# Kernel optimization log

Hardware: AMD Instinct MI355X
Metric: run time of the kernel (lower is better)

The kernel has to match this reference:

```python
import jax, jax.numpy as jnp
import numpy as np

NODES_PER_GRAPH = 116
HEADS = 2
D_HEAD = 116  # out_channels per head
HID = 256
B = 512
N = B * NODES_PER_GRAPH
DEG = 8
E = N * DEG
D_OUT = HEADS * D_HEAD  # 232


def setup_inputs() -> dict:
    key = jax.random.key(0)
    ks = jax.random.split(key, 6)
    h_flat = jax.random.normal(ks[0], (N, HID), dtype=jnp.float32)
    # every node receives DEG edges from random nodes within its own 116-node graph
    dst = jnp.repeat(jnp.arange(N, dtype=jnp.int64), DEG)
    offs = jax.random.randint(ks[1], (E,), 0, NODES_PER_GRAPH, dtype=jnp.int64)
    src = (dst // NODES_PER_GRAPH) * NODES_PER_GRAPH + offs
    edge_index = jnp.stack([src, dst], axis=0)
    batch_index = jnp.repeat(jnp.arange(B, dtype=jnp.int64), NODES_PER_GRAPH)
    s = 1.0 / np.sqrt(HID)
    Wq = jax.random.normal(ks[2], (HID, D_OUT), dtype=jnp.float32) * s
    Wk = jax.random.normal(ks[3], (HID, D_OUT), dtype=jnp.float32) * s
    Wv = jax.random.normal(ks[4], (HID, D_OUT), dtype=jnp.float32) * s
    Ws = jax.random.normal(ks[5], (HID, D_OUT), dtype=jnp.float32) * s
    return {"h_flat": h_flat, "edge_index": edge_index, "batch_index": batch_index,
            "Wq": Wq, "Wk": Wk, "Wv": Wv, "Ws": Ws}


def _graph_transformer_layer(h, edge_index, Wq, Wk, Wv, Ws):
    # PyG TransformerConv-style multi-head edge attention, concat heads + root skip.
    n = h.shape[0]
    q = (h @ Wq).reshape(n, HEADS, D_HEAD)
    k = (h @ Wk).reshape(n, HEADS, D_HEAD)
    v = (h @ Wv).reshape(n, HEADS, D_HEAD)
    src, dst = edge_index[0], edge_index[1]
    # per-edge scores [E, H]
    scores = jnp.einsum('ehd,ehd->eh', q[dst], k[src]) / np.sqrt(D_HEAD)
    # segment softmax over incoming edges of each dst node
    m = jax.ops.segment_max(scores, dst, num_segments=n)
    m = jnp.where(jnp.isfinite(m), m, 0.0)
    ex = jnp.exp(scores - m[dst])
    denom = jax.ops.segment_sum(ex, dst, num_segments=n)
    alpha_e = ex / (denom[dst] + 1e-16)
    msg = alpha_e[:, :, None] * v[src]                      # [E, H, Dh]
    attn = jax.ops.segment_sum(msg, dst, num_segments=n)    # [N, H, Dh]
    return attn.reshape(n, D_OUT) + h @ Ws


def reference(h_flat, edge_index, batch_index, Wq, Wk, Wv, Ws):
    n = h_flat.shape[0]
    b = n // NODES_PER_GRAPH
    h_proj = _graph_transformer_layer(h_flat, edge_index, Wq, Wk, Wv, Ws)  # [N, 232]
    e = h_proj.mean(axis=-1)                                 # [N]
    # scatter_softmax over per-graph node segments
    em = jax.ops.segment_max(e, batch_index, num_segments=b)
    ee = jnp.exp(e - em[batch_index])
    es = jax.ops.segment_sum(ee, batch_index, num_segments=b)
    alpha = ee / es[batch_index]                             # [N]
    h_weighted = alpha[:, None] * h_proj                     # [N, 232]
    alpha_map = alpha.reshape(b, NODES_PER_GRAPH)            # [B, 116]
    return alpha_map, h_weighted
```

## Files before the change

### kernel.cpp

```cpp
#include <hip/hip_runtime.h>

#define NODES  116
#define HEADS  2
#define DH     116
#define HID    256
#define NGRAPH 512
#define NN     (NGRAPH*NODES)
#define DEG    8
#define DOUT   (HEADS*DH)
#define RSTR   120

typedef short  s8v  __attribute__((ext_vector_type(8)));
typedef float  f4v  __attribute__((ext_vector_type(4)));

static __device__ __forceinline__ float bf2f(unsigned short u) {
    union { unsigned int i; float f; } c; c.i = ((unsigned int)u) << 16; return c.f;
}
static __device__ __forceinline__ unsigned short f2bf(float f) {
    union { float f; unsigned int u; } c; c.f = f;
    unsigned int u = c.u;
    unsigned int r = (u + 0x7FFFu + ((u >> 16) & 1u)) >> 16;
    return (unsigned short)r;
}

#define GLD_LDS16(gptr, lptr) \
    __builtin_amdgcn_global_load_lds((const __attribute__((address_space(1))) void*)(gptr), \
                                     (__attribute__((address_space(3))) void*)(lptr), 16, 0, 0)

__global__ __launch_bounds__(256) void prep_h(const float* __restrict__ h,
                                              unsigned short* __restrict__ hs)
{
    unsigned int f = blockIdx.x * 256 + threadIdx.x;
    unsigned int m    = f & 127;
    unsigned int quad = (f >> 7) & 3;
    unsigned int kb   = (f >> 9) & 7;
    unsigned int g    = f >> 12;
    unsigned short o[8] = {0,0,0,0,0,0,0,0};
    if (m < NODES) {
        unsigned int row = g * NODES + m;
        unsigned int k   = kb * 32 + quad * 8;
        const float4 v0 = *(const float4*)(h + (size_t)row * HID + k);
        const float4 v1 = *(const float4*)(h + (size_t)row * HID + k + 4);
        o[0]=f2bf(v0.x); o[1]=f2bf(v0.y); o[2]=f2bf(v0.z); o[3]=f2bf(v0.w);
        o[4]=f2bf(v1.x); o[5]=f2bf(v1.y); o[6]=f2bf(v1.z); o[7]=f2bf(v1.w);
    }
    *(uint4*)(hs + (size_t)f * 8) = *(const uint4*)o;
}

__global__ __launch_bounds__(256) void prep_w(const float* __restrict__ Wq,
                                              const float* __restrict__ Wk,
                                              const float* __restrict__ Wv,
                                              const float* __restrict__ Ws,
                                              unsigned short* __restrict__ wt)
{
    unsigned int f = blockIdx.x * 256 + threadIdx.x;
    unsigned int n    = f & 127;
    unsigned int quad = (f >> 7) & 3;
    unsigned int kb   = (f >> 9) & 7;
    unsigned int ch   = (f >> 12) & 3;
    unsigned int hd   = f >> 14;
    unsigned short o[8] = {0,0,0,0,0,0,0,0};
    if (n < NODES) {
        unsigned int col = hd * DH + n;
        unsigned int k   = kb * 32 + quad * 8;
        const float* W = (ch == 0) ? Wq : (ch == 1) ? Wk : (ch == 2) ? Wv : Ws;
        #pragma unroll
        for (int i = 0; i < 8; i++)
            o[i] = f2bf(W[(size_t)(k + i) * DOUT + col]);
    }
    *(uint4*)(wt + (size_t)f * 8) = *(const uint4*)o;
}

__global__ __launch_bounds__(1024) void fused_k1(const unsigned short* __restrict__ hs,
                                                 const unsigned short* __restrict__ wt,
                                                 const int* __restrict__ eidx,
                                                 unsigned short* __restrict__ hp,
                                                 float* __restrict__ psums)
{
    __shared__ unsigned short stA[2][4096];
    __shared__ unsigned short stB[2][4096];
    __shared__ unsigned short ql[NODES * RSTR];
    __shared__ unsigned short kl[NODES * RSTR];
    __shared__ unsigned short vl[NODES * RSTR];
    __shared__ unsigned short sl[NODES * RSTR];
    __shared__ int   srcl[NODES * DEG];
    __shared__ float alph[NODES * DEG];

    const int b   = blockIdx.x;
    const int g   = b & 511;
    const int hd  = b >> 9;
    const int tid = threadIdx.x;
    const int w    = tid >> 6;
    const int lane = tid & 63;
    const int l15  = lane & 15;
    const int quad = lane >> 4;
    const int wm   = w >> 2;
    const int wn   = w & 3;

    if (tid < NODES * DEG)
        srcl[tid] = eidx[(size_t)g * NODES * DEG + tid] - g * NODES;

    const char* gA = (const char*)(hs + (size_t)g * 32768);
    const char* gB = (const char*)(wt + (size_t)hd * 4 * 8 * 4096);

    #define ISSUE(s, buf) do {                                                   \
        int _kb = (s) & 7, _ch = (s) >> 3;                                       \
        if (w < 8) { GLD_LDS16(gA + _kb * 8192 + w * 1024 + lane * 16,           \
                               (char*)stA[buf] + w * 1024); }                    \
        else       { int _w8 = w - 8;                                            \
                     GLD_LDS16(gB + (_ch * 8 + _kb) * 8192 + _w8 * 1024 + lane * 16, \
                               (char*)stB[buf] + _w8 * 1024); }                  \
    } while (0)

    f4v acc[2][2];
    #pragma unroll
    for (int i = 0; i < 2; i++)
        #pragma unroll
        for (int j = 0; j < 2; j++)
            #pragma unroll
            for (int r = 0; r < 4; r++) acc[i][j][r] = 0.0f;

    ISSUE(0, 0);
    for (int s = 0; s < 32; s++) {
        __syncthreads();
        if (s < 31) ISSUE(s + 1, (s + 1) & 1);
        const unsigned short* A = stA[s & 1];
        const unsigned short* B = stB[s & 1];
        s8v a[2], bb[2];
        #pragma unroll
        for (int t = 0; t < 2; t++) {
            int m = wm * 32 + t * 16 + l15;
            a[t]  = *(const s8v*)(A + (quad * 128 + m) * 8);
            int n = wn * 32 + t * 16 + l15;
            bb[t] = *(const s8v*)(B + (quad * 128 + n) * 8);
        }
        #pragma unroll
        for (int i = 0; i < 2; i++)
            #pragma unroll
            for (int j = 0; j < 2; j++)
                acc[i][j] = __builtin_amdgcn_mfma_f32_16x16x32_bf16(a[i], bb[j], acc[i][j], 0, 0, 0);

        if ((s & 7) == 7) {
            int ch = s >> 3;
            unsigned short* dst = (ch == 0) ? ql : (ch == 1) ? kl : (ch == 2) ? vl : sl;
            #pragma unroll
            for (int i = 0; i < 2; i++) {
                #pragma unroll
                for (int j = 0; j < 2; j++) {
                    int col = wn * 32 + j * 16 + l15;
                    #pragma unroll
                    for (int r = 0; r < 4; r++) {
                        int row = wm * 32 + i * 16 + quad * 4 + r;
                        if (row < NODES && col < NODES)
                            dst[row * RSTR + col] = f2bf(acc[i][j][r]);
                        acc[i][j][r] = 0.0f;
                    }
                }
            }
        }
    }
    __syncthreads();

    if (tid < NODES * DEG) {
        const int i = tid >> 3;
        const int src = srcl[tid];
        float s = 0.0f;
        #pragma unroll 4
        for (int gi = 0; gi < 29; gi++) {
            uint2 qg = *(const uint2*)(ql + i * RSTR + gi * 4);
            uint2 kg = *(const uint2*)(kl + src * RSTR + gi * 4);
            s += bf2f((unsigned short)(qg.x & 0xFFFF)) * bf2f((unsigned short)(kg.x & 0xFFFF));
            s += bf2f((unsigned short)(qg.x >> 16))    * bf2f((unsigned short)(kg.x >> 16));
            s += bf2f((unsigned short)(qg.y & 0xFFFF)) * bf2f((unsigned short)(kg.y & 0xFFFF));
            s += bf2f((unsigned short)(qg.y >> 16))    * bf2f((unsigned short)(kg.y >> 16));
        }
        s *= 0.09284766908852594f;
        float m = s;
        m = fmaxf(m, __shfl_xor(m, 1));
        m = fmaxf(m, __shfl_xor(m, 2));
        m = fmaxf(m, __shfl_xor(m, 4));
        float e = __expf(s - m);
        float sum = e;
        sum += __shfl_xor(sum, 1);
        sum += __shfl_xor(sum, 2);
        sum += __shfl_xor(sum, 4);
        alph[tid] = e / sum;
    }
    __syncthreads();

    if (tid < NODES * DEG) {
        const int i  = tid >> 3;
        const int cs = tid & 7;
        float al[DEG]; int sj[DEG];
        #pragma unroll
        for (int j = 0; j < DEG; j++) { al[j] = alph[i * DEG + j]; sj[j] = srcl[i * DEG + j]; }
        float rsum = 0.0f;
        for (int c = cs; c < NODES; c += 8) {
            float v = bf2f(sl[i * RSTR + c]);
            #pragma unroll
            for (int j = 0; j < DEG; j++)
                v += al[j] * bf2f(vl[sj[j] * RSTR + c]);
            ql[i * RSTR + c] = f2bf(v);
            rsum += v;
        }
        rsum += __shfl_xor(rsum, 1);
        rsum += __shfl_xor(rsum, 2);
        rsum += __shfl_xor(rsum, 4);
        if (cs == 0) psums[((size_t)hd * NGRAPH + g) * NODES + i] = rsum;
    }
    __syncthreads();

    for (int f = tid; f < NODES * 29; f += 1024) {
        int r  = f / 29;
        int gi = f - r * 29;
        *(uint2*)(hp + ((size_t)(g * NODES + r)) * DOUT + hd * DH + gi * 4) =
            *(const uint2*)(ql + r * RSTR + gi * 4);
    }
    #undef ISSUE
}

__global__ __launch_bounds__(256) void pool_k2(const unsigned short* __restrict__ hp,
                                               const float* __restrict__ psums,
                                               float* __restrict__ out_alpha,
                                               float* __restrict__ out_hw)
{
    __shared__ float ew[NODES];
    __shared__ float alph[NODES];
    __shared__ float red[2];

    const int g   = blockIdx.x;
    const int tid = threadIdx.x;

    if (tid < NODES)
        ew[tid] = (psums[(size_t)g * NODES + tid] +
                   psums[((size_t)NGRAPH + g) * NODES + tid]) * (1.0f / DOUT);
    __syncthreads();
    if (tid < 64) {
        float a = ew[tid];
        float b = (tid + 64 < NODES) ? ew[tid + 64] : -1e30f;
        float mm = fmaxf(a, b);
        #pragma unroll
        for (int off = 32; off > 0; off >>= 1) mm = fmaxf(mm, __shfl_down(mm, off));
        if (tid == 0) red[0] = mm;
    }
    __syncthreads();
    if (tid < NODES) ew[tid] = __expf(ew[tid] - red[0]);
    __syncthreads();
    if (tid < 64) {
        float a = ew[tid] + ((tid + 64 < NODES) ? ew[tid + 64] : 0.0f);
        #pragma unroll
        for (int off = 32; off > 0; off >>= 1) a += __shfl_down(a, off);
        if (tid == 0) red[1] = a;
    }
    __syncthreads();
    if (tid < NODES) {
        float al = ew[tid] / red[1];
        alph[tid] = al;
        out_alpha[(size_t)g * NODES + tid] = al;
    }
    __syncthreads();

    for (int f = tid; f < NODES * 58; f += 256) {
        int r  = f / 58;
        int gi = f - r * 58;
        float al = alph[r];
        uint2 hv = *(const uint2*)(hp + ((size_t)(g * NODES + r)) * DOUT + gi * 4);
        float4 o = make_float4(al * bf2f((unsigned short)(hv.x & 0xFFFF)),
                               al * bf2f((unsigned short)(hv.x >> 16)),
                               al * bf2f((unsigned short)(hv.y & 0xFFFF)),
                               al * bf2f((unsigned short)(hv.y >> 16)));
        *(float4*)(out_hw + ((size_t)(g * NODES + r)) * DOUT + gi * 4) = o;
    }
}

extern "C" void kernel_launch(void* const* d_in, const int* in_sizes, int n_in,
                              void* d_out, int out_size, void* d_ws, size_t ws_size,
                              hipStream_t stream)
{
    const float* h    = (const float*)d_in[0];
    const int*   eidx = (const int*)d_in[1];
    const float* Wq   = (const float*)d_in[3];
    const float* Wk   = (const float*)d_in[4];
    const float* Wv   = (const float*)d_in[5];
    const float* Ws   = (const float*)d_in[6];

    unsigned short* hs = (unsigned short*)d_ws;
    unsigned short* wt = hs + (size_t)16777216;
    unsigned short* hp = wt + (size_t)262144;
    float*       psums = (float*)(hp + (size_t)13778944);

    float* out_alpha = (float*)d_out;
    float* out_hw    = out_alpha + NN;

    prep_h<<<8192, 256, 0, stream>>>(h, hs);
    prep_w<<<128, 256, 0, stream>>>(Wq, Wk, Wv, Ws, wt);
    fused_k1<<<1024, 1024, 0, stream>>>(hs, wt, eidx, hp, psums);
    pool_k2<<<NGRAPH, 256, 0, stream>>>(hp, psums, out_alpha, out_hw);
}
```

Before: 238.9 us.

## Fuse h bf16 conversion into GEMM and compute attention via dense MFMA

Removes the separate prep_h kernel; the fused kernel now reads fp32 h directly, converts it to bf16 and stages it in LDS, and loads all four weight chunks per k-step so Q/K/V/S accumulate at once. Edge scores become a dense 128x128 QK^T MFMA whose entries are gathered per edge, and the aggregation becomes a dense alpha-matrix times V MFMA that accumulates onto the skip term. The aim is to drop a full pass over h through global memory and replace scalar gather loops with tensor-core work. In exchange it loses the double-buffered async pipeline for A and adds redundant dense compute.

```diff
diff --git a/kernel.cpp b/kernel.cpp
--- a/kernel.cpp
+++ b/kernel.cpp
@@ -8,7 +8,7 @@
 #define NN     (NGRAPH*NODES)
 #define DEG    8
 #define DOUT   (HEADS*DH)
-#define RSTR   120
+#define RSTR   136
 
 typedef short  s8v  __attribute__((ext_vector_type(8)));
 typedef float  f4v  __attribute__((ext_vector_type(4)));
@@ -26,26 +26,6 @@
 #define GLD_LDS16(gptr, lptr) \
     __builtin_amdgcn_global_load_lds((const __attribute__((address_space(1))) void*)(gptr), \
                                      (__attribute__((address_space(3))) void*)(lptr), 16, 0, 0)
-
-__global__ __launch_bounds__(256) void prep_h(const float* __restrict__ h,
-                                              unsigned short* __restrict__ hs)
-{
-    unsigned int f = blockIdx.x * 256 + threadIdx.x;
-    unsigned int m    = f & 127;
-    unsigned int quad = (f >> 7) & 3;
-    unsigned int kb   = (f >> 9) & 7;
-    unsigned int g    = f >> 12;
-    unsigned short o[8] = {0,0,0,0,0,0,0,0};
-    if (m < NODES) {
-        unsigned int row = g * NODES + m;
-        unsigned int k   = kb * 32 + quad * 8;
-        const float4 v0 = *(const float4*)(h + (size_t)row * HID + k);
-        const float4 v1 = *(const float4*)(h + (size_t)row * HID + k + 4);
-        o[0]=f2bf(v0.x); o[1]=f2bf(v0.y); o[2]=f2bf(v0.z); o[3]=f2bf(v0.w);
-        o[4]=f2bf(v1.x); o[5]=f2bf(v1.y); o[6]=f2bf(v1.z); o[7]=f2bf(v1.w);
-    }
-    *(uint4*)(hs + (size_t)f * 8) = *(const uint4*)o;
-}
 
 __global__ __launch_bounds__(256) void prep_w(const float* __restrict__ Wq,
                                               const float* __restrict__ Wk,
@@ -71,20 +51,21 @@
     *(uint4*)(wt + (size_t)f * 8) = *(const uint4*)o;
 }
 
-__global__ __launch_bounds__(1024) void fused_k1(const unsigned short* __restrict__ hs,
-                                                 const unsigned short* __restrict__ wt,
-                                                 const int* __restrict__ eidx,
-                                                 unsigned short* __restrict__ hp,
-                                                 float* __restrict__ psums)
+__global__ __launch_bounds__(1024) void fused_gemm_attn(
+    const float* __restrict__ h,
+    const unsigned short* __restrict__ wt,
+    const int* __restrict__ eidx,
+    unsigned short* __restrict__ hp,
+    float* __restrict__ psums)
 {
-    __shared__ unsigned short stA[2][4096];
-    __shared__ unsigned short stB[2][4096];
-    __shared__ unsigned short ql[NODES * RSTR];
-    __shared__ unsigned short kl[NODES * RSTR];
-    __shared__ unsigned short vl[NODES * RSTR];
-    __shared__ unsigned short sl[NODES * RSTR];
-    __shared__ int   srcl[NODES * DEG];
-    __shared__ float alph[NODES * DEG];
+    __shared__ unsigned short stA[4096];
+    __shared__ unsigned short stB[4*4096];
+    __shared__ unsigned short ql[128*RSTR];
+    __shared__ unsigned short kl[128*RSTR];
+    __shared__ unsigned short vt[128*RSTR];
+    __shared__ int   srcl[NODES*DEG];
+    __shared__ float scf[NODES*DEG];
+    __shared__ float alph[NODES*DEG];
 
     const int b   = blockIdx.x;
     const int g   = b & 511;
@@ -100,61 +81,101 @@
     if (tid < NODES * DEG)
         srcl[tid] = eidx[(size_t)g * NODES * DEG + tid] - g * NODES;
 
-    const char* gA = (const char*)(hs + (size_t)g * 32768);
-    const char* gB = (const char*)(wt + (size_t)hd * 4 * 8 * 4096);
-
-    #define ISSUE(s, buf) do {                                                   \
-        int _kb = (s) & 7, _ch = (s) >> 3;                                       \
-        if (w < 8) { GLD_LDS16(gA + _kb * 8192 + w * 1024 + lane * 16,           \
-                               (char*)stA[buf] + w * 1024); }                    \
-        else       { int _w8 = w - 8;                                            \
-                     GLD_LDS16(gB + (_ch * 8 + _kb) * 8192 + _w8 * 1024 + lane * 16, \
-                               (char*)stB[buf] + _w8 * 1024); }                  \
-    } while (0)
-
-    f4v acc[2][2];
+    const int am  = tid >> 3;
+    const int q8  = tid & 7;
+    long grow = (long)g * NODES + am;
+    if (grow >= NN) grow = NN - 1;
+    const float* hrow = h + (size_t)grow * HID + q8 * 4;
+    unsigned short* aw = stA + ((q8 >> 1) * 128 + am) * 8 + (q8 & 1) * 4;
+
+    f4v accq[2][2], acck[2][2], accv[2][2], accs[2][2];
     #pragma unroll
     for (int i = 0; i < 2; i++)
         #pragma unroll
         for (int j = 0; j < 2; j++)
             #pragma unroll
-            for (int r = 0; r < 4; r++) acc[i][j][r] = 0.0f;
-
-    ISSUE(0, 0);
-    for (int s = 0; s < 32; s++) {
+            for (int r = 0; r < 4; r++) {
+                accq[i][j][r] = 0.f; acck[i][j][r] = 0.f;
+                accv[i][j][r] = 0.f; accs[i][j][r] = 0.f;
+            }
+
+    const size_t wbase = (size_t)hd * 4 * 8 * 4096;
+
+    for (int kb = 0; kb < 8; kb++) {
+        float4 av = *(const float4*)(hrow + kb * 32);
+        unsigned short o[4] = { f2bf(av.x), f2bf(av.y), f2bf(av.z), f2bf(av.w) };
+        *(uint2*)aw = *(const uint2*)o;
+        #pragma unroll
+        for (int j = 0; j < 2; j++) {
+            int c = w * 2 + j;
+            int ch = c >> 3, sub = c & 7;
+            const unsigned short* src = wt + wbase + ((size_t)(ch * 8 + kb)) * 4096 + sub * 512;
+            GLD_LDS16((const char*)src + lane * 16, (char*)stB + c * 1024);
+        }
         __syncthreads();
-        if (s < 31) ISSUE(s + 1, (s + 1) & 1);
-        const unsigned short* A = stA[s & 1];
-        const unsigned short* B = stB[s & 1];
-        s8v a[2], bb[2];
-        #pragma unroll
-        for (int t = 0; t < 2; t++) {
-            int m = wm * 32 + t * 16 + l15;
-            a[t]  = *(const s8v*)(A + (quad * 128 + m) * 8);
-            int n = wn * 32 + t * 16 + l15;
-            bb[t] = *(const s8v*)(B + (quad * 128 + n) * 8);
-        }
-        #pragma unroll
-        for (int i = 0; i < 2; i++)
+
+        s8v a0 = *(const s8v*)(stA + (quad * 128 + wm * 32 + l15) * 8);
+        s8v a1 = *(const s8v*)(stA + (quad * 128 + wm * 32 + 16 + l15) * 8);
+        #pragma unroll
+        for (int ch = 0; ch < 4; ch++) {
+            s8v b0 = *(const s8v*)(stB + ch * 4096 + (quad * 128 + wn * 32 + l15) * 8);
+            s8v b1 = *(const s8v*)(stB + ch * 4096 + (quad * 128 + wn * 32 + 16 + l15) * 8);
+            f4v (*acc)[2] = (ch == 0) ? accq : (ch == 1) ? acck : (ch == 2) ? accv : accs;
+            acc[0][0] = __builtin_amdgcn_mfma_f32_16x16x32_bf16(a0, b0, acc[0][0], 0, 0, 0);
+            acc[0][1] = __builtin_amdgcn_mfma_f32_16x16x32_bf16(a0, b1, acc[0][1], 0, 0, 0);
+            acc[1][0] = __builtin_amdgcn_mfma_f32_16x16x32_bf16(a1, b0, acc[1][0], 0, 0, 0);
+            acc[1][1] = __builtin_amdgcn_mfma_f32_16x16x32_bf16(a1, b1, acc[1][1], 0, 0, 0);
+        }
+        __syncthreads();
+    }
+
+    #pragma unroll
+    for (int i = 0; i < 2; i++) {
+        #pragma unroll
+        for (int j = 0; j < 2; j++) {
+            int col = wn * 32 + j * 16 + l15;
             #pragma unroll
-            for (int j = 0; j < 2; j++)
-                acc[i][j] = __builtin_amdgcn_mfma_f32_16x16x32_bf16(a[i], bb[j], acc[i][j], 0, 0, 0);
-
-        if ((s & 7) == 7) {
-            int ch = s >> 3;
-            unsigned short* dst = (ch == 0) ? ql : (ch == 1) ? kl : (ch == 2) ? vl : sl;
+            for (int r = 0; r < 4; r++) {
+                int row = wm * 32 + i * 16 + quad * 4 + r;
+                ql[row * RSTR + col] = (col < NODES) ? f2bf(accq[i][j][r]) : 0;
+                kl[row * RSTR + col] = (col < NODES) ? f2bf(acck[i][j][r]) : 0;
+                vt[col * RSTR + row] = (row < NODES) ? f2bf(accv[i][j][r]) : 0;
+            }
+        }
+    }
+    __syncthreads();
+
+    f4v sacc[2][2];
+    #pragma unroll
+    for (int i = 0; i < 2; i++)
+        #pragma unroll
+        for (int j = 0; j < 2; j++)
             #pragma unroll
-            for (int i = 0; i < 2; i++) {
+            for (int r = 0; r < 4; r++) sacc[i][j][r] = 0.f;
+    #pragma unroll
+    for (int ks = 0; ks < 4; ks++) {
+        s8v a0 = *(const s8v*)(ql + (wm * 32 + l15) * RSTR + ks * 32 + quad * 8);
+        s8v a1 = *(const s8v*)(ql + (wm * 32 + 16 + l15) * RSTR + ks * 32 + quad * 8);
+        s8v b0 = *(const s8v*)(kl + (wn * 32 + l15) * RSTR + ks * 32 + quad * 8);
+        s8v b1 = *(const s8v*)(kl + (wn * 32 + 16 + l15) * RSTR + ks * 32 + quad * 8);
+        sacc[0][0] = __builtin_amdgcn_mfma_f32_16x16x32_bf16(a0, b0, sacc[0][0], 0, 0, 0);
+        sacc[0][1] = __builtin_amdgcn_mfma_f32_16x16x32_bf16(a0, b1, sacc[0][1], 0, 0, 0);
+        sacc[1][0] = __builtin_amdgcn_mfma_f32_16x16x32_bf16(a1, b0, sacc[1][0], 0, 0, 0);
+        sacc[1][1] = __builtin_amdgcn_mfma_f32_16x16x32_bf16(a1, b1, sacc[1][1], 0, 0, 0);
+    }
+    #pragma unroll
+    for (int i = 0; i < 2; i++) {
+        #pragma unroll
+        for (int r = 0; r < 4; r++) {
+            int row = wm * 32 + i * 16 + quad * 4 + r;
+            if (row < NODES) {
                 #pragma unroll
                 for (int j = 0; j < 2; j++) {
                     int col = wn * 32 + j * 16 + l15;
                     #pragma unroll
-                    for (int r = 0; r < 4; r++) {
-                        int row = wm * 32 + i * 16 + quad * 4 + r;
-                        if (row < NODES && col < NODES)
-                            dst[row * RSTR + col] = f2bf(acc[i][j][r]);
-                        acc[i][j][r] = 0.0f;
-                    }
+                    for (int e = 0; e < DEG; e++)
+                        if (srcl[row * DEG + e] == col)
+                            scf[row * DEG + e] = sacc[i][j][r];
                 }
             }
         }
@@ -162,19 +183,7 @@
     __syncthreads();
 
     if (tid < NODES * DEG) {
-        const int i = tid >> 3;
-        const int src = srcl[tid];
-        float s = 0.0f;
-        #pragma unroll 4
-        for (int gi = 0; gi < 29; gi++) {
-            uint2 qg = *(const uint2*)(ql + i * RSTR + gi * 4);
-            uint2 kg = *(const uint2*)(kl + src * RSTR + gi * 4);
-            s += bf2f((unsigned short)(qg.x & 0xFFFF)) * bf2f((unsigned short)(kg.x & 0xFFFF));
-            s += bf2f((unsigned short)(qg.x >> 16))    * bf2f((unsigned short)(kg.x >> 16));
-            s += bf2f((unsigned short)(qg.y & 0xFFFF)) * bf2f((unsigned short)(kg.y & 0xFFFF));
-            s += bf2f((unsigned short)(qg.y >> 16))    * bf2f((unsigned short)(kg.y >> 16));
-        }
-        s *= 0.09284766908852594f;
+        float s = scf[tid] * 0.09284766908852594f;
         float m = s;
         m = fmaxf(m, __shfl_xor(m, 1));
         m = fmaxf(m, __shfl_xor(m, 2));
@@ -186,37 +195,78 @@
         sum += __shfl_xor(sum, 4);
         alph[tid] = e / sum;
     }
+    for (int f = tid; f < 128 * RSTR / 4; f += 1024)
+        *(uint2*)(kl + f * 4) = make_uint2(0u, 0u);
+    __syncthreads();
+
+    if (tid < NODES) {
+        #pragma unroll
+        for (int j = 0; j < DEG; j++) {
+            int sj = srcl[tid * DEG + j];
+            bool first = true;
+            for (int jj = 0; jj < j; jj++) first = first && (srcl[tid * DEG + jj] != sj);
+            if (first) {
+                float a = alph[tid * DEG + j];
+                for (int jj = j + 1; jj < DEG; jj++)
+                    if (srcl[tid * DEG + jj] == sj) a += alph[tid * DEG + jj];
+                kl[tid * RSTR + sj] = f2bf(a);
+            }
+        }
+    }
+    __syncthreads();
+
+    #pragma unroll
+    for (int ks = 0; ks < 4; ks++) {
+        s8v a0 = *(const s8v*)(kl + (wm * 32 + l15) * RSTR + ks * 32 + quad * 8);
+        s8v a1 = *(const s8v*)(kl + (wm * 32 + 16 + l15) * RSTR + ks * 32 + quad * 8);
+        s8v b0 = *(const s8v*)(vt + (wn * 32 + l15) * RSTR + ks * 32 + quad * 8);
+        s8v b1 = *(const s8v*)(vt + (wn * 32 + 16 + l15) * RSTR + ks * 32 + quad * 8);
+        accs[0][0] = __builtin_amdgcn_mfma_f32_16x16x32_bf16(a0, b0, accs[0][0], 0, 0, 0);
+        accs[0][1] = __builtin_amdgcn_mfma_f32_16x16x32_bf16(a0, b1, accs[0][1], 0, 0, 0);
+        accs[1][0] = __builtin_amdgcn_mfma_f32_16x16x32_bf16(a1, b0, accs[1][0], 0, 0, 0);
+        accs[1][1] = __builtin_amdgcn_mfma_f32_16x16x32_bf16(a1, b1, accs[1][1], 0, 0, 0);
+    }
+    __syncthreads();
+
+    unsigned short* hpl = vt;
+    #pragma unroll
+    for (int i = 0; i < 2; i++) {
+        #pragma unroll
+        for (int j = 0; j < 2; j++) {
+            int col = wn * 32 + j * 16 + l15;
+            #pragma unroll
+            for (int r = 0; r < 4; r++) {
+                int row = wm * 32 + i * 16 + quad * 4 + r;
+                hpl[row * RSTR + col] = f2bf(accs[i][j][r]);
+            }
+        }
+    }
     __syncthreads();
 
     if (tid < NODES * DEG) {
         const int i  = tid >> 3;
-        const int cs = tid & 7;
-        float al[DEG]; int sj[DEG];
-        #pragma unroll
-        for (int j = 0; j < DEG; j++) { al[j] = alph[i * DEG + j]; sj[j] = srcl[i * DEG + j]; }
-        float rsum = 0.0f;
-        for (int c = cs; c < NODES; c += 8) {
-            float v = bf2f(sl[i * RSTR + c]);
-            #pragma unroll
-            for (int j = 0; j < DEG; j++)
-                v += al[j] * bf2f(vl[sj[j] * RSTR + c]);
-            ql[i * RSTR + c] = f2bf(v);
-            rsum += v;
-        }
-        rsum += __shfl_xor(rsum, 1);
-        rsum += __shfl_xor(rsum, 2);
-        rsum += __shfl_xor(rsum, 4);
-        if (cs == 0) psums[((size_t)hd * NGRAPH + g) * NODES + i] = rsum;
-    }
-    __syncthreads();
-
+        const int seg = tid & 7;
+        float rs = 0.0f;
+        #pragma unroll
+        for (int t = 0; t < 2; t++) {
+            int gi = seg + t * 8;
+            if (gi < 15) {
+                const s8v v8 = *(const s8v*)(hpl + i * RSTR + gi * 8);
+                #pragma unroll
+                for (int e = 0; e < 8; e++) rs += bf2f(((unsigned short*)&v8)[e]);
+            }
+        }
+        rs += __shfl_xor(rs, 1);
+        rs += __shfl_xor(rs, 2);
+        rs += __shfl_xor(rs, 4);
+        if (seg == 0) psums[((size_t)hd * NGRAPH + g) * NODES + i] = rs;
+    }
     for (int f = tid; f < NODES * 29; f += 1024) {
         int r  = f / 29;
         int gi = f - r * 29;
         *(uint2*)(hp + ((size_t)(g * NODES + r)) * DOUT + hd * DH + gi * 4) =
-            *(const uint2*)(ql + r * RSTR + gi * 4);
-    }
-    #undef ISSUE
+            *(const uint2*)(hpl + r * RSTR + gi * 4);
+    }
 }
 
 __global__ __launch_bounds__(256) void pool_k2(const unsigned short* __restrict__ hp,
@@ -284,16 +334,14 @@
     const float* Wv   = (const float*)d_in[5];
     const float* Ws   = (const float*)d_in[6];
 
-    unsigned short* hs = (unsigned short*)d_ws;
-    unsigned short* wt = hs + (size_t)16777216;
+    unsigned short* wt = (unsigned short*)d_ws;
     unsigned short* hp = wt + (size_t)262144;
     float*       psums = (float*)(hp + (size_t)13778944);
 
     float* out_alpha = (float*)d_out;
     float* out_hw    = out_alpha + NN;
 
-    prep_h<<<8192, 256, 0, stream>>>(h, hs);
     prep_w<<<128, 256, 0, stream>>>(Wq, Wk, Wv, Ws, wt);
-    fused_k1<<<1024, 1024, 0, stream>>>(hs, wt, eidx, hp, psums);
+    fused_gemm_attn<<<1024, 1024, 0, stream>>>(h, wt, eidx, hp, psums);
     pool_k2<<<NGRAPH, 256, 0, stream>>>(hp, psums, out_alpha, out_hw);
 }
```

New measurement: 217.7 us. 1.1x faster.
